# Kernel tuning notes

Measured on AMD Instinct MI355X. Metric: run time of the kernel, lower is better.

The kernel has to match this reference:

```python
import jax, jax.numpy as jnp
import numpy as np
from math import sqrt

D_MODEL, D_COND, N_HEADS = 512, 768, 8
B, H, W, L_COND = 8, 64, 64, 256


def setup_inputs() -> dict:
    key = jax.random.key(0)
    ks = jax.random.split(key, 7)
    return {
        "image": jax.random.normal(ks[0], (B, D_MODEL, H, W), jnp.float32),
        "cond": jax.random.normal(ks[1], (B, L_COND, D_COND), jnp.float32),
        "attention_mask": jnp.zeros((B, H * W, L_COND), jnp.float32),
        "Wq": jax.random.normal(ks[2], (D_MODEL, D_MODEL), jnp.float32) * 0.02,
        "Wk": jax.random.normal(ks[3], (D_MODEL, D_COND), jnp.float32) * 0.02,
        "Wv": jax.random.normal(ks[4], (D_MODEL, D_COND), jnp.float32) * 0.02,
        "Wo": jax.random.normal(ks[5], (D_MODEL, D_MODEL), jnp.float32) * 0.02,
        "bo": jnp.zeros((D_MODEL,), jnp.float32),
    }


def reference(image, cond, attention_mask, Wq, Wk, Wv, Wo, bo):
    b, d, h, w = image.shape
    L = h * w
    n = N_HEADS
    dh = d // n
    scale = sqrt(dh)
    # b d h w -> b l d
    x = image.reshape(b, d, L).transpose(0, 2, 1)
    # projections (torch Linear: y = x @ W.T), split heads: b l (n dh) -> b n l dh
    q = (x @ Wq.T).reshape(b, L, n, dh).transpose(0, 2, 1, 3)
    k = (cond @ Wk.T).reshape(b, -1, n, dh).transpose(0, 2, 1, 3)
    v = (cond @ Wv.T).reshape(b, -1, n, dh).transpose(0, 2, 1, 3)
    attn = jnp.einsum("bnqd,bnkd->bnqk", q, k) / scale
    attn = attn + attention_mask[:, None]  # b 1 L L_cond
    p = jax.nn.softmax(attn, axis=-1)
    o = jnp.einsum("bnqk,bnkd->bnqd", p, v)  # b n L dh
    # b n (h w) dh -> b (n dh) h w
    o = o.transpose(0, 1, 3, 2).reshape(b, d, h, w)
    # 1x1 conv == per-pixel linear over channels
    out = jnp.einsum("oc,bchw->bohw", Wo, o) + bo[None, :, None, None]
    return out
```

## Files before the change

### kernel.cpp

```cpp
#include <hip/hip_runtime.h>

typedef __bf16 bf16x8 __attribute__((ext_vector_type(8)));
typedef float f32x4 __attribute__((ext_vector_type(4)));
typedef short s4 __attribute__((ext_vector_type(4)));
typedef unsigned short ush;

#define DEV __device__ __forceinline__


DEV ush f2bf(float x){
  union { float f; unsigned u; } v; v.f = x;
  unsigned r = v.u + 0x7FFFu + ((v.u >> 16) & 1u);
  return (ush)(r >> 16);
}

DEV short bfcast(float x){
  union { __bf16 h; short s; } cv; cv.h = (__bf16)x; return cv.s;
}

DEV void gload_lds16(const ush* g, ush* l){
  __builtin_amdgcn_global_load_lds(
      (const __attribute__((address_space(1))) unsigned int*)g,
      (__attribute__((address_space(3))) unsigned int*)l, 16, 0, 0);
}

__global__ __launch_bounds__(256) void tc_kernel(const float* __restrict__ img, ush* __restrict__ xT){
  __shared__ float tile[32][33];
  const int b = blockIdx.z;
  const int l0 = blockIdx.x << 5, c0 = blockIdx.y << 5;
  const int tx = threadIdx.x & 31, ty = threadIdx.x >> 5;
  const float* src = img + ((size_t)b*512 + c0)*4096 + l0;
  #pragma unroll
  for (int i = 0; i < 32; i += 8) tile[ty+i][tx] = src[(size_t)(ty+i)*4096 + tx];
  __syncthreads();
  ush* dst = xT + ((size_t)b*4096 + l0)*512 + c0;
  #pragma unroll
  for (int i = 0; i < 32; i += 8) dst[(size_t)(ty+i)*512 + tx] = f2bf(tile[tx][ty+i]);
}

__global__ __launch_bounds__(256) void cvt_kernel(const float* c0,const float* c1,const float* c2,
                                                  const float* c3,const float* c4,
                                                  ush* o0, ush* o1, ush* o2, ush* o3, ush* o4){
  const int N0=1572864, N1=262144, N2=393216, N3=393216, N4=262144;
  const int stride = gridDim.x * blockDim.x;
  for (int i = blockIdx.x*blockDim.x + threadIdx.x; i < N0+N1+N2+N3+N4; i += stride){
    int j = i; const float* s; ush* d;
    if (j < N0){ s=c0; d=o0; }
    else { j-=N0; if (j<N1){s=c1;d=o1;}
      else { j-=N1; if (j<N2){s=c2;d=o2;}
        else { j-=N2; if (j<N3){s=c3;d=o3;} else { j-=N3; s=c4; d=o4; } } } }
    d[j] = f2bf(s[j]);
  }
}

DEV void gemm_core(const ush* __restrict__ Ag, long long a_row0, int lda,
                   const ush* __restrict__ Bg, long long b_row0, int ldb,
                   int K, ush* As, ush* Bs, f32x4 acc[4][4])
{
  const int t = threadIdx.x;
  const int lane = t & 63;
  const int wid = t >> 6, wr = wid >> 1, wc = wid & 1;
  #pragma unroll
  for (int mt=0;mt<4;mt++)
    #pragma unroll
    for (int nt=0;nt<4;nt++) acc[mt][nt] = f32x4{0.f,0.f,0.f,0.f};

  const int nk = K >> 6;
  for (int kt = 0; kt < nk; ++kt){
    const int k0 = kt << 6;
    #pragma unroll
    for (int r = 0; r < 4; ++r){
      int idx = (r<<8) + t;
      int row = idx >> 3, slot = idx & 7;
      gload_lds16(Ag + (a_row0 + row)*(long long)lda + k0 + ((slot ^ (row&7))<<3), As + idx*8);
    }
    #pragma unroll
    for (int r = 0; r < 4; ++r){
      int idx = (r<<8) + t;
      int row = idx >> 3, slot = idx & 7;
      gload_lds16(Bg + (b_row0 + row)*(long long)ldb + k0 + ((slot ^ (row&7))<<3), Bs + idx*8);
    }
    __syncthreads();
    #pragma unroll
    for (int kk = 0; kk < 2; ++kk){
      bf16x8 af[4], bfv[4];
      #pragma unroll
      for (int mt=0;mt<4;mt++){
        int row = (wr<<6) + (mt<<4) + (lane & 15);
        int byte = (row<<7) + (kk<<6) + ((lane>>4)<<4);
        byte ^= (row & 7) << 4;
        af[mt] = *(const bf16x8*)((const char*)As + byte);
      }
      #pragma unroll
      for (int nt=0;nt<4;nt++){
        int row = (wc<<6) + (nt<<4) + (lane & 15);
        int byte = (row<<7) + (kk<<6) + ((lane>>4)<<4);
        byte ^= (row & 7) << 4;
        bfv[nt] = *(const bf16x8*)((const char*)Bs + byte);
      }
      #pragma unroll
      for (int mt=0;mt<4;mt++)
        #pragma unroll
        for (int nt=0;nt<4;nt++)
          acc[mt][nt] = __builtin_amdgcn_mfma_f32_16x16x32_bf16(af[mt], bfv[nt], acc[mt][nt], 0,0,0);
    }
    __syncthreads();
  }
}

__global__ __launch_bounds__(256,2) void qproj_kernel(const ush* __restrict__ xT, const ush* __restrict__ Wqb,
                                                      ush* __restrict__ Qg){
  __shared__ ush As[8192], Bs[8192];
  f32x4 acc[4][4];
  const int nb = blockIdx.x & 3, mb = blockIdx.x >> 2;
  gemm_core(xT, (long long)mb*128, 512, Wqb, (long long)nb*128, 512, 512, As, Bs, acc);
  const int lane = threadIdx.x & 63, wid = threadIdx.x >> 6, wr = wid>>1, wc = wid&1;
  #pragma unroll
  for (int mt=0;mt<4;mt++)
    #pragma unroll
    for (int nt=0;nt<4;nt++)
      #pragma unroll
      for (int r=0;r<4;r++){
        int m = mb*128 + (wr<<6) + (mt<<4) + ((lane>>4)<<2) + r;
        int n = (nb<<7) + (wc<<6) + (nt<<4) + (lane&15);
        int bb = m >> 12, l = m & 4095, hh = n >> 6, dh = n & 63;
        Qg[(((size_t)(bb*8 + hh)*4096 + l)<<6) + dh] = f2bf(acc[mt][nt][r] * 0.125f);
      }
}

__global__ __launch_bounds__(256,2) void kvproj_kernel(const ush* __restrict__ cb, const ush* __restrict__ Wkb,
                                                       const ush* __restrict__ Wvb, ush* __restrict__ Kg,
                                                       ush* __restrict__ Vt){
  __shared__ ush As[8192], Bs[8192];
  f32x4 acc[4][4];
  const int which = blockIdx.z;
  const int nb = blockIdx.x & 3, mb = blockIdx.x >> 2;
  gemm_core(cb, (long long)mb*128, 768, which ? Wvb : Wkb, (long long)nb*128, 768, 768, As, Bs, acc);
  const int lane = threadIdx.x & 63, wid = threadIdx.x >> 6, wr = wid>>1, wc = wid&1;
  #pragma unroll
  for (int mt=0;mt<4;mt++)
    #pragma unroll
    for (int nt=0;nt<4;nt++)
      #pragma unroll
      for (int r=0;r<4;r++){
        int m = mb*128 + (wr<<6) + (mt<<4) + ((lane>>4)<<2) + r;
        int n = (nb<<7) + (wc<<6) + (nt<<4) + (lane&15);
        int bb = m >> 8, j = m & 255;
        ush val = f2bf(acc[mt][nt][r]);
        if (!which) Kg[(((size_t)(bb*256 + j))<<9) + n] = val;
        else { int hh = n>>6, dh = n&63; Vt[(((size_t)((bb*8+hh)*64 + dh))<<8) + j] = val; }
      }
}

__global__ __launch_bounds__(512,2) void attn_kernel(const ush* __restrict__ Qg, const ush* __restrict__ Kg,
                                                     const ush* __restrict__ Vg, const float* __restrict__ mask,
                                                     ush* __restrict__ Oc){
  extern __shared__ char smem[];
  ush* Ks = (ush*)smem;
  ush* Vs = (ush*)(smem + 32768);
  const int t = threadIdx.x, lane = t & 63, wid = t >> 6;
  const int qb = blockIdx.x, h = blockIdx.y, b = blockIdx.z;

  #pragma unroll
  for (int r = 0; r < 4; ++r){
    int idx = (r<<9) + t;
    int j = idx >> 3, slot = idx & 7;
    gload_lds16(Kg + ((size_t)(b*256 + j))*512 + h*64 + ((slot ^ (j&7))<<3), Ks + idx*8);
  }
  #pragma unroll
  for (int r = 0; r < 4; ++r){
    int idx = (r<<9) + t;
    int dh = idx >> 5, slot = idx & 31;
    gload_lds16(Vg + ((size_t)((b*8 + h)*64 + dh))*256 + ((((slot&7) ^ (dh&7)) | (slot&24))<<3), Vs + idx*8);
  }
  __syncthreads();

  const int l15 = lane & 15, kg = lane >> 4;
  const int q0 = qb*512 + wid*64;
  const ush* Qbase = Qg + ((size_t)(b*8 + h)*4096)*64;

  #pragma unroll 1
  for (int mt = 0; mt < 4; ++mt){
    const int qg = q0 + mt*16 + l15;
    bf16x8 qf0 = *(const bf16x8*)(Qbase + (size_t)qg*64 + (kg<<3));
    bf16x8 qf1 = *(const bf16x8*)(Qbase + (size_t)qg*64 + 32 + (kg<<3));
    const float* mrow = mask + ((size_t)b*4096 + qg)*256 + (kg<<2);

    f32x4 oacc[4];
    #pragma unroll
    for (int tl=0;tl<4;++tl) oacc[tl] = f32x4{0.f,0.f,0.f,0.f};
    float m_run = 0.f;
    f32x4 svec = f32x4{0.f,0.f,0.f,0.f};

    #pragma unroll
    for (int hf = 0; hf < 2; ++hf){
      f32x4 sacc[8];
      #pragma unroll
      for (int nt=0;nt<8;++nt) sacc[nt] = f32x4{0.f,0.f,0.f,0.f};
      #pragma unroll
      for (int nt=0;nt<8;++nt){
        int row = (hf<<7) + (nt<<4) + l15;
        const char* kb = (const char*)Ks + (row<<7);
        int sw = (row&7)<<4;
        bf16x8 kf0 = *(const bf16x8*)(kb + ((kg<<4) ^ sw));
        bf16x8 kf1 = *(const bf16x8*)(kb + (((kg<<4)+64) ^ sw));
        sacc[nt] = __builtin_amdgcn_mfma_f32_16x16x32_bf16(kf0, qf0, sacc[nt], 0,0,0);
        sacc[nt] = __builtin_amdgcn_mfma_f32_16x16x32_bf16(kf1, qf1, sacc[nt], 0,0,0);
      }

      float mx = -3.0e38f;
      #pragma unroll
      for (int nt=0;nt<8;++nt){
        float4 mv = *(const float4*)(mrow + (hf<<7) + (nt<<4));
        sacc[nt][0] += mv.x; sacc[nt][1] += mv.y; sacc[nt][2] += mv.z; sacc[nt][3] += mv.w;
        #pragma unroll
        for (int r=0;r<4;++r) mx = fmaxf(mx, sacc[nt][r]);
      }
      mx = fmaxf(mx, __shfl_xor(mx, 16, 64));
      mx = fmaxf(mx, __shfl_xor(mx, 32, 64));

      if (hf == 0){
        m_run = mx;
      } else {
        float mnew = fmaxf(m_run, mx);
        float alpha = __expf(m_run - mnew);
        #pragma unroll
        for (int r=0;r<4;++r) svec[r] *= alpha;
        #pragma unroll
        for (int tl=0;tl<4;++tl)
          #pragma unroll
          for (int r=0;r<4;++r) oacc[tl][r] *= alpha;
        m_run = mnew;
      }

      #pragma unroll
      for (int nt=0;nt<8;++nt){
        s4 pf;
        #pragma unroll
        for (int r=0;r<4;++r){
          float p = __expf(sacc[nt][r] - m_run);
          svec[r] += p;
          pf[r] = bfcast(p);
        }
        #pragma unroll
        for (int tl=0;tl<4;++tl){
          int dr = (tl<<4) + l15;
          int off = ((hf<<8) + (nt<<5) + (kg<<3)) ^ ((dr&7)<<4);
          s4 vf = *(const s4*)((const char*)Vs + (dr<<9) + off);
          oacc[tl] = __builtin_amdgcn_mfma_f32_16x16x16bf16_1k(vf, pf, oacc[tl], 0,0,0);
        }
      }
      __builtin_amdgcn_sched_barrier(0);
    }

    float s_run = (svec[0] + svec[1]) + (svec[2] + svec[3]);
    s_run += __shfl_xor(s_run, 16, 64);
    s_run += __shfl_xor(s_run, 32, 64);
    const float rl = 1.f / s_run;
    #pragma unroll
    for (int tl=0;tl<4;++tl){
      s4 ov;
      #pragma unroll
      for (int r=0;r<4;++r) ov[r] = bfcast(oacc[tl][r] * rl);
      *(s4*)(Oc + (((size_t)b*4096 + qg)<<9) + h*64 + (tl<<4) + (kg<<2)) = ov;
    }
  }
}

__global__ __launch_bounds__(256,2) void oproj_kernel(const ush* __restrict__ Wob, const ush* __restrict__ Oc,
                                                      const float* __restrict__ bo, float* __restrict__ out){
  __shared__ ush As[8192], Bs[8192];
  f32x4 acc[4][4];
  const int bz = blockIdx.z;
  const int mb = blockIdx.x >> 5, nb = blockIdx.x & 31;
  gemm_core(Wob, (long long)mb*128, 512, Oc + (size_t)bz*4096*512, (long long)nb*128, 512, 512, As, Bs, acc);
  const int lane = threadIdx.x & 63, wid = threadIdx.x >> 6, wr = wid>>1, wc = wid&1;
  #pragma unroll
  for (int mt=0;mt<4;mt++)
    #pragma unroll
    for (int nt=0;nt<4;nt++){
      #pragma unroll
      for (int r=0;r<4;r++){
        int m = (mb<<7) + (wr<<6) + (mt<<4) + ((lane>>4)<<2) + r;
        int n = (nb<<7) + (wc<<6) + (nt<<4) + (lane&15);
        out[(((size_t)(bz*512 + m))<<12) + n] = acc[mt][nt][r] + bo[m];
      }
    }
}

extern "C" void kernel_launch(void* const* d_in, const int* in_sizes, int n_in,
                              void* d_out, int out_size, void* d_ws, size_t ws_size,
                              hipStream_t stream){
  const float* image = (const float*)d_in[0];
  const float* cond  = (const float*)d_in[1];
  const float* mask  = (const float*)d_in[2];
  const float* Wq    = (const float*)d_in[3];
  const float* Wk    = (const float*)d_in[4];
  const float* Wv    = (const float*)d_in[5];
  const float* Wo    = (const float*)d_in[6];
  const float* bo    = (const float*)d_in[7];
  float* out = (float*)d_out;

  char* ws = (char*)d_ws;
  ush* xT   = (ush*)(ws);
  ush* Oc   = xT;
  ush* Qg   = (ush*)(ws + 33554432);
  ush* cndb = (ush*)(ws + 67108864);
  ush* Kg   = (ush*)(ws + 70254592);
  ush* Vt   = (ush*)(ws + 72351744);
  ush* Wqb  = (ush*)(ws + 74448896);
  ush* Wkb  = (ush*)(ws + 74973184);
  ush* Wvb  = (ush*)(ws + 75759616);
  ush* Wob  = (ush*)(ws + 76546048);

  (void)hipFuncSetAttribute((const void*)attn_kernel,
                            hipFuncAttributeMaxDynamicSharedMemorySize, 65536);

  tc_kernel<<<dim3(128,16,8), 256, 0, stream>>>(image, xT);
  cvt_kernel<<<dim3(1024), 256, 0, stream>>>(cond, Wq, Wk, Wv, Wo, cndb, Wqb, Wkb, Wvb, Wob);
  qproj_kernel<<<dim3(1024), 256, 0, stream>>>(xT, Wqb, Qg);
  kvproj_kernel<<<dim3(64,1,2), 256, 0, stream>>>(cndb, Wkb, Wvb, Kg, Vt);
  attn_kernel<<<dim3(8,8,8), 512, 65536, stream>>>(Qg, Kg, Vt, mask, Oc);
  oproj_kernel<<<dim3(128,1,8), 256, 0, stream>>>(Wob, Oc, bo, out);
}
```

Measured before the change: 161.0 us.

## Process two query tiles per wave sharing K/V fragments, double block size

```diff
diff --git a/kernel.cpp b/kernel.cpp
--- a/kernel.cpp
+++ b/kernel.cpp
@@ -152,9 +152,9 @@
       }
 }
 
-__global__ __launch_bounds__(512,2) void attn_kernel(const ush* __restrict__ Qg, const ush* __restrict__ Kg,
-                                                     const ush* __restrict__ Vg, const float* __restrict__ mask,
-                                                     ush* __restrict__ Oc){
+__global__ __launch_bounds__(1024,3) void attn_kernel(const ush* __restrict__ Qg, const ush* __restrict__ Kg,
+                                                      const ush* __restrict__ Vg, const float* __restrict__ mask,
+                                                      ush* __restrict__ Oc){
   extern __shared__ char smem[];
   ush* Ks = (ush*)smem;
   ush* Vs = (ush*)(smem + 32768);
@@ -162,107 +162,121 @@
   const int qb = blockIdx.x, h = blockIdx.y, b = blockIdx.z;
 
   #pragma unroll
-  for (int r = 0; r < 4; ++r){
-    int idx = (r<<9) + t;
+  for (int r = 0; r < 2; ++r){
+    int idx = (r<<10) + t;
     int j = idx >> 3, slot = idx & 7;
     gload_lds16(Kg + ((size_t)(b*256 + j))*512 + h*64 + ((slot ^ (j&7))<<3), Ks + idx*8);
   }
   #pragma unroll
-  for (int r = 0; r < 4; ++r){
-    int idx = (r<<9) + t;
+  for (int r = 0; r < 2; ++r){
+    int idx = (r<<10) + t;
     int dh = idx >> 5, slot = idx & 31;
     gload_lds16(Vg + ((size_t)((b*8 + h)*64 + dh))*256 + ((((slot&7) ^ (dh&7)) | (slot&24))<<3), Vs + idx*8);
   }
   __syncthreads();
 
   const int l15 = lane & 15, kg = lane >> 4;
-  const int q0 = qb*512 + wid*64;
   const ush* Qbase = Qg + ((size_t)(b*8 + h)*4096)*64;
+  const int q00 = qb*1024 + wid*64;
 
   #pragma unroll 1
-  for (int mt = 0; mt < 4; ++mt){
-    const int qg = q0 + mt*16 + l15;
-    bf16x8 qf0 = *(const bf16x8*)(Qbase + (size_t)qg*64 + (kg<<3));
-    bf16x8 qf1 = *(const bf16x8*)(Qbase + (size_t)qg*64 + 32 + (kg<<3));
-    const float* mrow = mask + ((size_t)b*4096 + qg)*256 + (kg<<2);
-
-    f32x4 oacc[4];
-    #pragma unroll
-    for (int tl=0;tl<4;++tl) oacc[tl] = f32x4{0.f,0.f,0.f,0.f};
-    float m_run = 0.f;
-    f32x4 svec = f32x4{0.f,0.f,0.f,0.f};
-
-    #pragma unroll
-    for (int hf = 0; hf < 2; ++hf){
-      f32x4 sacc[8];
-      #pragma unroll
-      for (int nt=0;nt<8;++nt) sacc[nt] = f32x4{0.f,0.f,0.f,0.f};
-      #pragma unroll
-      for (int nt=0;nt<8;++nt){
-        int row = (hf<<7) + (nt<<4) + l15;
+  for (int mp = 0; mp < 2; ++mp){
+    const int qA = q00 + mp*32 + l15;
+    const int qB = qA + 16;
+    bf16x8 qf00 = *(const bf16x8*)(Qbase + (size_t)qA*64 + (kg<<3));
+    bf16x8 qf01 = *(const bf16x8*)(Qbase + (size_t)qA*64 + 32 + (kg<<3));
+    bf16x8 qf10 = *(const bf16x8*)(Qbase + (size_t)qB*64 + (kg<<3));
+    bf16x8 qf11 = *(const bf16x8*)(Qbase + (size_t)qB*64 + 32 + (kg<<3));
+    const float* mrowA = mask + ((size_t)b*4096 + qA)*256 + (kg<<2);
+    const float* mrowB = mrowA + (16<<8);
+
+    f32x4 oaccA[4], oaccB[4];
+    #pragma unroll
+    for (int tl=0;tl<4;++tl){ oaccA[tl] = f32x4{0.f,0.f,0.f,0.f}; oaccB[tl] = f32x4{0.f,0.f,0.f,0.f}; }
+    float mA = 0.f, mB = 0.f;
+    f32x4 svA = f32x4{0.f,0.f,0.f,0.f}, svB = f32x4{0.f,0.f,0.f,0.f};
+
+    #pragma unroll 1
+    for (int qt = 0; qt < 4; ++qt){
+      f32x4 sA[4], sB[4];
+      #pragma unroll
+      for (int nt=0;nt<4;++nt){ sA[nt] = f32x4{0.f,0.f,0.f,0.f}; sB[nt] = f32x4{0.f,0.f,0.f,0.f}; }
+      #pragma unroll
+      for (int nt=0;nt<4;++nt){
+        int row = (qt<<6) + (nt<<4) + l15;
         const char* kb = (const char*)Ks + (row<<7);
         int sw = (row&7)<<4;
         bf16x8 kf0 = *(const bf16x8*)(kb + ((kg<<4) ^ sw));
         bf16x8 kf1 = *(const bf16x8*)(kb + (((kg<<4)+64) ^ sw));
-        sacc[nt] = __builtin_amdgcn_mfma_f32_16x16x32_bf16(kf0, qf0, sacc[nt], 0,0,0);
-        sacc[nt] = __builtin_amdgcn_mfma_f32_16x16x32_bf16(kf1, qf1, sacc[nt], 0,0,0);
-      }
-
-      float mx = -3.0e38f;
-      #pragma unroll
-      for (int nt=0;nt<8;++nt){
-        float4 mv = *(const float4*)(mrow + (hf<<7) + (nt<<4));
-        sacc[nt][0] += mv.x; sacc[nt][1] += mv.y; sacc[nt][2] += mv.z; sacc[nt][3] += mv.w;
-        #pragma unroll
-        for (int r=0;r<4;++r) mx = fmaxf(mx, sacc[nt][r]);
-      }
-      mx = fmaxf(mx, __shfl_xor(mx, 16, 64));
-      mx = fmaxf(mx, __shfl_xor(mx, 32, 64));
-
-      if (hf == 0){
-        m_run = mx;
+        sA[nt] = __builtin_amdgcn_mfma_f32_16x16x32_bf16(kf0, qf00, sA[nt], 0,0,0);
+        sA[nt] = __builtin_amdgcn_mfma_f32_16x16x32_bf16(kf1, qf01, sA[nt], 0,0,0);
+        sB[nt] = __builtin_amdgcn_mfma_f32_16x16x32_bf16(kf0, qf10, sB[nt], 0,0,0);
+        sB[nt] = __builtin_amdgcn_mfma_f32_16x16x32_bf16(kf1, qf11, sB[nt], 0,0,0);
+      }
+
+      float mxA = -3.0e38f, mxB = -3.0e38f;
+      #pragma unroll
+      for (int nt=0;nt<4;++nt){
+        float4 va = *(const float4*)(mrowA + (qt<<6) + (nt<<4));
+        float4 vb = *(const float4*)(mrowB + (qt<<6) + (nt<<4));
+        sA[nt][0]+=va.x; sA[nt][1]+=va.y; sA[nt][2]+=va.z; sA[nt][3]+=va.w;
+        sB[nt][0]+=vb.x; sB[nt][1]+=vb.y; sB[nt][2]+=vb.z; sB[nt][3]+=vb.w;
+        #pragma unroll
+        for (int r=0;r<4;++r){ mxA = fmaxf(mxA, sA[nt][r]); mxB = fmaxf(mxB, sB[nt][r]); }
+      }
+      mxA = fmaxf(mxA, __shfl_xor(mxA, 16, 64));
+      mxA = fmaxf(mxA, __shfl_xor(mxA, 32, 64));
+      mxB = fmaxf(mxB, __shfl_xor(mxB, 16, 64));
+      mxB = fmaxf(mxB, __shfl_xor(mxB, 32, 64));
+
+      if (qt == 0){
+        mA = mxA; mB = mxB;
       } else {
-        float mnew = fmaxf(m_run, mx);
-        float alpha = __expf(m_run - mnew);
-        #pragma unroll
-        for (int r=0;r<4;++r) svec[r] *= alpha;
+        float mnA = fmaxf(mA, mxA), mnB = fmaxf(mB, mxB);
+        float aA = __expf(mA - mnA), aB = __expf(mB - mnB);
+        #pragma unroll
+        for (int r=0;r<4;++r){ svA[r] *= aA; svB[r] *= aB; }
         #pragma unroll
         for (int tl=0;tl<4;++tl)
           #pragma unroll
-          for (int r=0;r<4;++r) oacc[tl][r] *= alpha;
-        m_run = mnew;
-      }
-
-      #pragma unroll
-      for (int nt=0;nt<8;++nt){
-        s4 pf;
+          for (int r=0;r<4;++r){ oaccA[tl][r] *= aA; oaccB[tl][r] *= aB; }
+        mA = mnA; mB = mnB;
+      }
+
+      #pragma unroll
+      for (int nt=0;nt<4;++nt){
+        s4 pA, pB;
         #pragma unroll
         for (int r=0;r<4;++r){
-          float p = __expf(sacc[nt][r] - m_run);
-          svec[r] += p;
-          pf[r] = bfcast(p);
+          float pa = __expf(sA[nt][r] - mA);
+          float pb = __expf(sB[nt][r] - mB);
+          svA[r] += pa; svB[r] += pb;
+          pA[r] = bfcast(pa); pB[r] = bfcast(pb);
         }
         #pragma unroll
         for (int tl=0;tl<4;++tl){
           int dr = (tl<<4) + l15;
-          int off = ((hf<<8) + (nt<<5) + (kg<<3)) ^ ((dr&7)<<4);
+          int off = ((qt<<7) + (nt<<5) + (kg<<3)) ^ ((dr&7)<<4);
           s4 vf = *(const s4*)((const char*)Vs + (dr<<9) + off);
-          oacc[tl] = __builtin_amdgcn_mfma_f32_16x16x16bf16_1k(vf, pf, oacc[tl], 0,0,0);
+          oaccA[tl] = __builtin_amdgcn_mfma_f32_16x16x16bf16_1k(vf, pA, oaccA[tl], 0,0,0);
+          oaccB[tl] = __builtin_amdgcn_mfma_f32_16x16x16bf16_1k(vf, pB, oaccB[tl], 0,0,0);
         }
       }
       __builtin_amdgcn_sched_barrier(0);
     }
 
-    float s_run = (svec[0] + svec[1]) + (svec[2] + svec[3]);
-    s_run += __shfl_xor(s_run, 16, 64);
-    s_run += __shfl_xor(s_run, 32, 64);
-    const float rl = 1.f / s_run;
+    float sAt = (svA[0]+svA[1]) + (svA[2]+svA[3]);
+    float sBt = (svB[0]+svB[1]) + (svB[2]+svB[3]);
+    sAt += __shfl_xor(sAt, 16, 64); sAt += __shfl_xor(sAt, 32, 64);
+    sBt += __shfl_xor(sBt, 16, 64); sBt += __shfl_xor(sBt, 32, 64);
+    const float rlA = 1.f / sAt, rlB = 1.f / sBt;
     #pragma unroll
     for (int tl=0;tl<4;++tl){
-      s4 ov;
-      #pragma unroll
-      for (int r=0;r<4;++r) ov[r] = bfcast(oacc[tl][r] * rl);
-      *(s4*)(Oc + (((size_t)b*4096 + qg)<<9) + h*64 + (tl<<4) + (kg<<2)) = ov;
+      s4 ovA, ovB;
+      #pragma unroll
+      for (int r=0;r<4;++r){ ovA[r] = bfcast(oaccA[tl][r] * rlA); ovB[r] = bfcast(oaccB[tl][r] * rlB); }
+      *(s4*)(Oc + (((size_t)b*4096 + qA)<<9) + h*64 + (tl<<4) + (kg<<2)) = ovA;
+      *(s4*)(Oc + (((size_t)b*4096 + qB)<<9) + h*64 + (tl<<4) + (kg<<2)) = ovB;
     }
   }
 }
@@ -320,6 +334,6 @@
   cvt_kernel<<<dim3(1024), 256, 0, stream>>>(cond, Wq, Wk, Wv, Wo, cndb, Wqb, Wkb, Wvb, Wob);
   qproj_kernel<<<dim3(1024), 256, 0, stream>>>(xT, Wqb, Qg);
   kvproj_kernel<<<dim3(64,1,2), 256, 0, stream>>>(cndb, Wkb, Wvb, Kg, Vt);
-  attn_kernel<<<dim3(8,8,8), 512, 65536, stream>>>(Qg, Kg, Vt, mask, Oc);
+  attn_kernel<<<dim3(4,8,8), 1024, 65536, stream>>>(Qg, Kg, Vt, mask, Oc);
   oproj_kernel<<<dim3(128,1,8), 256, 0, stream>>>(Wob, Oc, bo, out);
 }
```

Measured after the change: 159.0 us. Within noise of the previous version (-1.3%).
